# Kernel tuning notes

Measured on AMD Instinct MI355X. Metric: run time of the kernel, lower is better.

Reference implementation:

```python
import jax, jax.numpy as jnp
import numpy as np

NUM_USERS = 100000
NUM_ITEMS = 50000
NUM_NODES = NUM_USERS + NUM_ITEMS
EMBED_DIM = 128
NUM_LAYERS = 3
CONTENT_DIM = 768
NUM_EDGES = 1000000
BATCH = 4096
LAMBDA_CONTENT = 0.1
INIT_STD = 0.1


def setup_inputs() -> dict:
    key = jax.random.key(0)
    ks = jax.random.split(key, 9)
    edge_index = jax.random.randint(ks[0], (2, NUM_EDGES), 0, NUM_NODES, dtype=jnp.int64 if jax.config.jax_enable_x64 else jnp.int32)
    edge_weight = jax.random.uniform(ks[1], (NUM_EDGES,), dtype=jnp.float32)
    batch_users = jax.random.randint(ks[2], (BATCH,), 0, NUM_USERS)
    batch_pos_items = jax.random.randint(ks[3], (BATCH,), 0, NUM_ITEMS)
    batch_neg_items = jax.random.randint(ks[4], (BATCH,), 0, NUM_ITEMS)
    item_content = jax.random.normal(ks[5], (NUM_ITEMS, CONTENT_DIM), dtype=jnp.float32)
    user_emb_w = INIT_STD * jax.random.normal(ks[6], (NUM_USERS, EMBED_DIM), dtype=jnp.float32)
    item_emb_w = INIT_STD * jax.random.normal(ks[7], (NUM_ITEMS, EMBED_DIM), dtype=jnp.float32)
    # nn.Linear(item_content_dim, embed_dim, bias=False): weight [embed_dim, content_dim]
    bound = 1.0 / np.sqrt(CONTENT_DIM)
    content_proj_w = jax.random.uniform(ks[8], (EMBED_DIM, CONTENT_DIM), minval=-bound, maxval=bound, dtype=jnp.float32)
    return {
        'edge_index': edge_index, 'edge_weight': edge_weight,
        'batch_users': batch_users, 'batch_pos_items': batch_pos_items,
        'batch_neg_items': batch_neg_items, 'item_content': item_content,
        'user_emb_w': user_emb_w, 'item_emb_w': item_emb_w,
        'content_proj_w': content_proj_w,
    }


def _lgconv(x, src, dst, ew, num_nodes):
    # PyG LGConv: gcn_norm(add_self_loops=False) then scatter-add at target.
    deg = jax.ops.segment_sum(ew, dst, num_segments=num_nodes)          # [N]
    dinv = jnp.where(deg > 0, jax.lax.rsqrt(deg), 0.0)
    norm = dinv[src] * ew * dinv[dst]                                    # [E]
    return jax.ops.segment_sum(norm[:, None] * x[src], dst, num_segments=num_nodes)


def _propagate(user_emb_w, item_emb_w, src, dst, ew):
    x = jnp.concatenate([user_emb_w, item_emb_w], axis=0)               # [N, D]
    acc = x
    for _ in range(NUM_LAYERS):
        x = _lgconv(x, src, dst, ew, NUM_NODES)
        acc = acc + x
    x_final = acc / (NUM_LAYERS + 1)
    return x_final[:NUM_USERS], x_final[NUM_USERS:]


def reference(edge_index, edge_weight, batch_users, batch_pos_items,
              batch_neg_items, item_content, user_emb_w, item_emb_w,
              content_proj_w):
    src, dst = edge_index[0], edge_index[1]
    u_final, i_final = _propagate(user_emb_w, item_emb_w, src, dst, edge_weight)
    u = u_final[batch_users]
    i_pos = i_final[batch_pos_items]
    i_neg = i_final[batch_neg_items]
    pos_score = jnp.sum(u * i_pos, axis=-1)
    neg_score = jnp.sum(u * i_neg, axis=-1)
    bpr = jnp.mean(jax.nn.softplus(-(pos_score - neg_score)))
    reg = jnp.mean(jnp.sum(u**2, axis=1) + jnp.sum(i_pos**2, axis=1) + jnp.sum(i_neg**2, axis=1)) * 1e-4
    proj = item_content @ content_proj_w.T                              # [I, D]
    align = jnp.mean((i_final - proj) ** 2)
    loss = bpr + reg + LAMBDA_CONTENT * align
    return loss, u_final, i_final
```

## Files before the change

kernel.cpp:

```cpp
#include <hip/hip_runtime.h>
#include <math.h>

#define NU 100000
#define NI 50000
#define NN 150000
#define D 128
#define NE 1000000
#define CD 768
#define BATCH 4096
#define NGEMM 782
#define NGB ((NN + 31) / 32)
#define NK (CD / 64)

typedef short bf16x8 __attribute__((ext_vector_type(8)));
typedef float f32x4 __attribute__((ext_vector_type(4)));

static inline size_t alignup(size_t x, size_t a) { return (x + a - 1) / a * a; }

__device__ inline unsigned short f2bf(float f) {
  unsigned int u = __builtin_bit_cast(unsigned int, f);
  unsigned int r = (u + 0x7fffu + ((u >> 16) & 1u)) >> 16;
  return (unsigned short)r;
}
__device__ inline unsigned int pack2bf(float lo, float hi) {
  return (unsigned int)f2bf(lo) | ((unsigned int)f2bf(hi) << 16);
}
__device__ inline float bflo(unsigned int p) {
  return __builtin_bit_cast(float, p << 16);
}
__device__ inline float bfhi(unsigned int p) {
  return __builtin_bit_cast(float, p & 0xffff0000u);
}

#define ACC8(P, W)                                                        \
  a[0] = fmaf(W, bflo(P.x), a[0]); a[1] = fmaf(W, bfhi(P.x), a[1]);       \
  a[2] = fmaf(W, bflo(P.y), a[2]); a[3] = fmaf(W, bfhi(P.y), a[3]);       \
  a[4] = fmaf(W, bflo(P.z), a[4]); a[5] = fmaf(W, bfhi(P.z), a[5]);       \
  a[6] = fmaf(W, bflo(P.w), a[6]); a[7] = fmaf(W, bfhi(P.w), a[7]);

__device__ __forceinline__ void gather_rows(
    const int* __restrict__ row_ptr, const int* __restrict__ csrc,
    const float* __restrict__ cnorm, const uint4* __restrict__ xin,
    int n, int sub, float* a) {
  int beg = row_ptr[n], end = row_ptr[n + 1];
  int j = beg;
  for (; j + 4 <= end; j += 4) {
    int s0 = csrc[j], s1 = csrc[j + 1], s2 = csrc[j + 2], s3 = csrc[j + 3];
    float w0 = cnorm[j], w1 = cnorm[j + 1], w2 = cnorm[j + 2], w3 = cnorm[j + 3];
    uint4 p0 = xin[(size_t)s0 * 16 + sub];
    uint4 p1 = xin[(size_t)s1 * 16 + sub];
    uint4 p2 = xin[(size_t)s2 * 16 + sub];
    uint4 p3 = xin[(size_t)s3 * 16 + sub];
    ACC8(p0, w0) ACC8(p1, w1) ACC8(p2, w2) ACC8(p3, w3)
  }
  for (; j < end; ++j) {
    int s0 = csrc[j];
    float w0 = cnorm[j];
    uint4 p0 = xin[(size_t)s0 * 16 + sub];
    ACC8(p0, w0)
  }
}

__global__ __launch_bounds__(512) void prep_kernel(
    const int* __restrict__ dst, int* __restrict__ cnt, int* __restrict__ cpos,
    const float* __restrict__ uemb, const float* __restrict__ iemb,
    unsigned int* __restrict__ x0b) {
  int sub = blockIdx.x;
  int half = sub >> 1;
  int tid = threadIdx.x;
  if ((sub & 1) == 0) {
    int i = half * 512 + tid;
    for (; i < NE; i += 1024 * 512)
      cpos[i] = atomicAdd(&cnt[dst[i]], 1);
  } else {
    const size_t XT = (size_t)NN * D / 8;
    size_t t = (size_t)half * 512 + tid;
    for (; t < XT; t += (size_t)1024 * 512) {
      size_t f = t * 8;
      const float* p = (f < (size_t)NU * D) ? (uemb + f) : (iemb + (f - (size_t)NU * D));
      float4 a = *(const float4*)p;
      float4 b = *(const float4*)(p + 4);
      uint4 o;
      o.x = pack2bf(a.x, a.y); o.y = pack2bf(a.z, a.w);
      o.z = pack2bf(b.x, b.y); o.w = pack2bf(b.z, b.w);
      *(uint4*)(x0b + t * 4) = o;
    }
  }
}


__global__ void scan_p1(const int* __restrict__ cnt, int* __restrict__ bsum) {
  __shared__ int s[256];
  int b = blockIdx.x;
  int i = b * 256 + threadIdx.x;
  s[threadIdx.x] = (i < NN) ? cnt[i] : 0;
  __syncthreads();
  for (int off = 128; off; off >>= 1) {
    if (threadIdx.x < off) s[threadIdx.x] += s[threadIdx.x + off];
    __syncthreads();
  }
  if (threadIdx.x == 0) bsum[b] = s[0];
}

__global__ __launch_bounds__(1024) void scan_p2(int* __restrict__ bsum, int nb) {
  __shared__ int s[1024];
  int t = threadIdx.x;
  int v = (t < nb) ? bsum[t] : 0;
  s[t] = v;
  __syncthreads();
  for (int off = 1; off < 1024; off <<= 1) {
    int u = (t >= off) ? s[t - off] : 0;
    __syncthreads();
    s[t] += u;
    __syncthreads();
  }
  if (t < nb) bsum[t] = s[t] - v;
}

__global__ void scan_p3(const int* __restrict__ cnt, const int* __restrict__ bsum,
                        int* __restrict__ row_ptr) {
  __shared__ int s[256];
  int b = blockIdx.x;
  int i = b * 256 + threadIdx.x;
  s[threadIdx.x] = (i < NN) ? cnt[i] : 0;
  __syncthreads();
  for (int off = 1; off < 256; off <<= 1) {
    int t = (threadIdx.x >= off) ? s[threadIdx.x - off] : 0;
    __syncthreads();
    s[threadIdx.x] += t;
    __syncthreads();
  }
  if (i < NN) row_ptr[i + 1] = bsum[b] + s[threadIdx.x];
  if (i == 0) row_ptr[0] = 0;
}

__global__ void fill_kernel(const int* __restrict__ src, const int* __restrict__ dst,
                            const float* __restrict__ ew, const int* __restrict__ row_ptr,
                            const int* __restrict__ cpos, int* __restrict__ csrc,
                            float* __restrict__ cew) {
  int i = blockIdx.x * blockDim.x + threadIdx.x;
  int stride = gridDim.x * blockDim.x;
  for (; i < NE; i += stride) {
    int p = row_ptr[dst[i]] + cpos[i];
    csrc[p] = src[i];
    cew[p] = ew[i];
  }
}

__global__ void degrow_kernel(const int* __restrict__ row_ptr, const float* __restrict__ cew,
                              float* __restrict__ dinv) {
  int n = blockIdx.x * blockDim.x + threadIdx.x;
  if (n >= NN) return;
  int beg = row_ptr[n], end = row_ptr[n + 1];
  float s = 0.f;
  for (int p = beg; p < end; ++p) s += cew[p];
  dinv[n] = (s > 0.f) ? rsqrtf(s) : 0.f;
}

__global__ void norm_kernel(const int* __restrict__ csrc, const float* __restrict__ cew,
                            const float* __restrict__ dinv, float* __restrict__ cnorm) {
  int i = blockIdx.x * blockDim.x + threadIdx.x;
  int stride = gridDim.x * blockDim.x;
  for (; i < NE; i += stride) cnorm[i] = dinv[csrc[i]] * cew[i];
}

__global__ __launch_bounds__(512) void gather1_gemm_kernel(
    const int* __restrict__ row_ptr, const int* __restrict__ csrc,
    const float* __restrict__ cnorm, const float* __restrict__ dinv,
    const uint4* __restrict__ x0b, uint4* __restrict__ y1b,
    const float* __restrict__ W, const float* __restrict__ content,
    uint4* __restrict__ proj) {
  __shared__ unsigned short Asm[64 * 64];
  __shared__ unsigned short Bsm[128 * 64];

  int bid = blockIdx.x;
  int tid = threadIdx.x;

  if (bid >= NGEMM) {
    int wv = tid >> 6, lane = tid & 63;
    int g = lane >> 4, sub = lane & 15;
    int n = (bid - NGEMM) * 32 + wv * 4 + g;
    if (n >= NN) return;
    float a[8] = {0.f, 0.f, 0.f, 0.f, 0.f, 0.f, 0.f, 0.f};
    gather_rows(row_ptr, csrc, cnorm, x0b, n, sub, a);
    float sc = dinv[n];
    uint4 o;
    o.x = pack2bf(a[0] * sc, a[1] * sc);
    o.y = pack2bf(a[2] * sc, a[3] * sc);
    o.z = pack2bf(a[4] * sc, a[5] * sc);
    o.w = pack2bf(a[6] * sc, a[7] * sc);
    y1b[(size_t)n * 16 + sub] = o;
    return;
  }

  int w = tid >> 6, lane = tid & 63;
  int i0 = bid * 64;
  int lrow = lane & 15, kq = lane >> 4;

  f32x4 acc[4];
#pragma unroll
  for (int rt = 0; rt < 4; ++rt) acc[rt] = (f32x4){0.f, 0.f, 0.f, 0.f};

  int sr = tid >> 3, c8 = tid & 7;
  int arow_g = (i0 + sr < NI) ? (i0 + sr) : (NI - 1);
  const float* aG = content + (size_t)arow_g * CD + c8 * 8;
  const float* bG0 = W + (size_t)sr * CD + c8 * 8;
  const float* bG1 = W + (size_t)(sr + 64) * CD + c8 * 8;
  int aoff = (c8 * 16) ^ ((sr & 7) << 4);

  {
    float4 a0 = *(const float4*)(aG);
    float4 a1 = *(const float4*)(aG + 4);
    float4 p0 = *(const float4*)(bG0);
    float4 p1 = *(const float4*)(bG0 + 4);
    float4 q0 = *(const float4*)(bG1);
    float4 q1 = *(const float4*)(bG1 + 4);
    uint4 oa, ob, oc;
    oa.x = pack2bf(a0.x, a0.y); oa.y = pack2bf(a0.z, a0.w);
    oa.z = pack2bf(a1.x, a1.y); oa.w = pack2bf(a1.z, a1.w);
    ob.x = pack2bf(p0.x, p0.y); ob.y = pack2bf(p0.z, p0.w);
    ob.z = pack2bf(p1.x, p1.y); ob.w = pack2bf(p1.z, p1.w);
    oc.x = pack2bf(q0.x, q0.y); oc.y = pack2bf(q0.z, q0.w);
    oc.z = pack2bf(q1.x, q1.y); oc.w = pack2bf(q1.z, q1.w);
    *(uint4*)((char*)Asm + sr * 128 + aoff) = oa;
    *(uint4*)((char*)Bsm + sr * 128 + aoff) = ob;
    *(uint4*)((char*)Bsm + (sr + 64) * 128 + aoff) = oc;
  }
  __syncthreads();

  for (int kk = 0; kk < NK; ++kk) {
    bool more = kk < NK - 1;
    float4 a0, a1, p0, p1, q0, q1;
    if (more) {
      int k0 = (kk + 1) * 64;
      a0 = *(const float4*)(aG + k0);
      a1 = *(const float4*)(aG + k0 + 4);
      p0 = *(const float4*)(bG0 + k0);
      p1 = *(const float4*)(bG0 + k0 + 4);
      q0 = *(const float4*)(bG1 + k0);
      q1 = *(const float4*)(bG1 + k0 + 4);
    }
#pragma unroll
    for (int ks = 0; ks < 2; ++ks) {
      int kbyte = ks * 64 + kq * 16;
      bf16x8 af[4], bfr;
#pragma unroll
      for (int rt = 0; rt < 4; ++rt) {
        int row = rt * 16 + lrow;
        af[rt] = *(const bf16x8*)((char*)Asm + row * 128 + (kbyte ^ ((row & 7) << 4)));
      }
      {
        int row = w * 16 + lrow;
        bfr = *(const bf16x8*)((char*)Bsm + row * 128 + (kbyte ^ ((row & 7) << 4)));
      }
#pragma unroll
      for (int rt = 0; rt < 4; ++rt)
        acc[rt] = __builtin_amdgcn_mfma_f32_16x16x32_bf16(af[rt], bfr, acc[rt], 0, 0, 0);
    }
    __syncthreads();
    if (more) {
      uint4 oa, ob, oc;
      oa.x = pack2bf(a0.x, a0.y); oa.y = pack2bf(a0.z, a0.w);
      oa.z = pack2bf(a1.x, a1.y); oa.w = pack2bf(a1.z, a1.w);
      ob.x = pack2bf(p0.x, p0.y); ob.y = pack2bf(p0.z, p0.w);
      ob.z = pack2bf(p1.x, p1.y); ob.w = pack2bf(p1.z, p1.w);
      oc.x = pack2bf(q0.x, q0.y); oc.y = pack2bf(q0.z, q0.w);
      oc.z = pack2bf(q1.x, q1.y); oc.w = pack2bf(q1.z, q1.w);
      *(uint4*)((char*)Asm + sr * 128 + aoff) = oa;
      *(uint4*)((char*)Bsm + sr * 128 + aoff) = ob;
      *(uint4*)((char*)Bsm + (sr + 64) * 128 + aoff) = oc;
      __syncthreads();
    }
  }

  unsigned short* T = (unsigned short*)Bsm;
  int dcol = w * 16 + lrow;
#pragma unroll
  for (int rt = 0; rt < 4; ++rt)
#pragma unroll
    for (int j = 0; j < 4; ++j)
      T[(rt * 16 + kq * 4 + j) * 128 + dcol] = f2bf(acc[rt][j]);
  __syncthreads();
#pragma unroll
  for (int u0 = 0; u0 < 2; ++u0) {
    int u = u0 * 512 + tid;
    int r = u >> 4, s = u & 15;
    int it = i0 + r;
    if (it < NI) proj[(size_t)it * 16 + s] = ((const uint4*)T)[u];
  }
}

__global__ __launch_bounds__(256) void gather_kernel(
    const int* __restrict__ row_ptr, const int* __restrict__ csrc,
    const float* __restrict__ cnorm, const float* __restrict__ dinv,
    const uint4* __restrict__ xin, uint4* __restrict__ yout) {
  int tid = threadIdx.x;
  int wv = tid >> 6, lane = tid & 63;
  int g = lane >> 4, sub = lane & 15;
  int n = blockIdx.x * 16 + wv * 4 + g;
  if (n >= NN) return;
  float a[8] = {0.f, 0.f, 0.f, 0.f, 0.f, 0.f, 0.f, 0.f};
  gather_rows(row_ptr, csrc, cnorm, xin, n, sub, a);
  float sc = dinv[n];
  uint4 o;
  o.x = pack2bf(a[0] * sc, a[1] * sc);
  o.y = pack2bf(a[2] * sc, a[3] * sc);
  o.z = pack2bf(a[4] * sc, a[5] * sc);
  o.w = pack2bf(a[6] * sc, a[7] * sc);
  yout[(size_t)n * 16 + sub] = o;
}

__global__ __launch_bounds__(256) void final_kernel(
    const int* __restrict__ row_ptr, const int* __restrict__ csrc,
    const float* __restrict__ cnorm, const float* __restrict__ dinv,
    const uint4* __restrict__ x0b, const uint4* __restrict__ y1b,
    const uint4* __restrict__ y2b, const uint4* __restrict__ proj,
    float* __restrict__ OUT, float* __restrict__ partials) {
  __shared__ float wred[4];
  int tid = threadIdx.x;
  int wv = tid >> 6, lane = tid & 63;
  int g = lane >> 4, sub = lane & 15;
  int n = blockIdx.x * 16 + wv * 4 + g;
  if (n >= NN) return;
  float a[8] = {0.f, 0.f, 0.f, 0.f, 0.f, 0.f, 0.f, 0.f};
  gather_rows(row_ptr, csrc, cnorm, y2b, n, sub, a);
  float sc = dinv[n];
  size_t r = (size_t)n * 16 + sub;
  uint4 q0 = x0b[r], q1 = y1b[r], q2 = y2b[r];
  float v[8];
  v[0] = (bflo(q0.x) + bflo(q1.x) + bflo(q2.x) + a[0] * sc) * 0.25f;
  v[1] = (bfhi(q0.x) + bfhi(q1.x) + bfhi(q2.x) + a[1] * sc) * 0.25f;
  v[2] = (bflo(q0.y) + bflo(q1.y) + bflo(q2.y) + a[2] * sc) * 0.25f;
  v[3] = (bfhi(q0.y) + bfhi(q1.y) + bfhi(q2.y) + a[3] * sc) * 0.25f;
  v[4] = (bflo(q0.z) + bflo(q1.z) + bflo(q2.z) + a[4] * sc) * 0.25f;
  v[5] = (bfhi(q0.z) + bfhi(q1.z) + bfhi(q2.z) + a[5] * sc) * 0.25f;
  v[6] = (bflo(q0.w) + bflo(q1.w) + bflo(q2.w) + a[6] * sc) * 0.25f;
  v[7] = (bfhi(q0.w) + bfhi(q1.w) + bfhi(q2.w) + a[7] * sc) * 0.25f;
  float* op = OUT + (size_t)n * D + sub * 8;
#pragma unroll
  for (int k = 0; k < 8; ++k) op[k] = v[k];

  if (blockIdx.x >= (NU / 16)) {
    uint4 pj = proj[(size_t)(n - NU) * 16 + sub];
    float d0 = v[0] - bflo(pj.x), d1 = v[1] - bfhi(pj.x);
    float d2 = v[2] - bflo(pj.y), d3 = v[3] - bfhi(pj.y);
    float d4 = v[4] - bflo(pj.z), d5 = v[5] - bfhi(pj.z);
    float d6 = v[6] - bflo(pj.w), d7 = v[7] - bfhi(pj.w);
    float m = d0 * d0 + d1 * d1 + d2 * d2 + d3 * d3 + d4 * d4 + d5 * d5 + d6 * d6 + d7 * d7;
    for (int off = 32; off; off >>= 1) m += __shfl_down(m, off);
    if (lane == 0) wred[wv] = m;
    __syncthreads();
    if (tid == 0)
      atomicAdd(&partials[blockIdx.x & 255], wred[0] + wred[1] + wred[2] + wred[3]);
  }
}

__global__ __launch_bounds__(256) void loss_batch(
    const int* __restrict__ bu, const int* __restrict__ bp, const int* __restrict__ bn,
    const float* __restrict__ OUT, float* __restrict__ accums) {
  __shared__ float wsp[4], wrg[4];
  int wv = threadIdx.x >> 6, lane = threadIdx.x & 63;
  int gw = blockIdx.x * 4 + wv;
  int nw = gridDim.x * 4;
  float lsp = 0.f, lrg = 0.f;
  for (int b = gw; b < BATCH; b += nw) {
    const float* u = OUT + (size_t)bu[b] * D;
    const float* ip = OUT + ((size_t)NU + bp[b]) * D;
    const float* in_ = OUT + ((size_t)NU + bn[b]) * D;
    float u0 = u[lane], u1 = u[lane + 64];
    float p0 = ip[lane], p1 = ip[lane + 64];
    float n0 = in_[lane], n1 = in_[lane + 64];
    float ps = u0 * p0 + u1 * p1;
    float ns = u0 * n0 + u1 * n1;
    float rg = u0 * u0 + u1 * u1 + p0 * p0 + p1 * p1 + n0 * n0 + n1 * n1;
    for (int off = 32; off; off >>= 1) {
      ps += __shfl_down(ps, off);
      ns += __shfl_down(ns, off);
      rg += __shfl_down(rg, off);
    }
    if (lane == 0) {
      float x = ns - ps;
      lsp += fmaxf(x, 0.f) + log1pf(expf(-fabsf(x)));
      lrg += rg;
    }
  }
  if (lane == 0) { wsp[wv] = lsp; wrg[wv] = lrg; }
  __syncthreads();
  if (threadIdx.x == 0) {
    atomicAdd(&accums[0], wsp[0] + wsp[1] + wsp[2] + wsp[3]);
    atomicAdd(&accums[1], wrg[0] + wrg[1] + wrg[2] + wrg[3]);
  }
}

__global__ void finalize_kernel(const float* __restrict__ accums,
                                const float* __restrict__ partials,
                                float* __restrict__ out0) {
  __shared__ float sm[4];
  int tid = threadIdx.x;
  float v = partials[tid];
  for (int off = 32; off; off >>= 1) v += __shfl_down(v, off);
  if ((tid & 63) == 0) sm[tid >> 6] = v;
  __syncthreads();
  if (tid == 0) {
    float align_sum = sm[0] + sm[1] + sm[2] + sm[3];
    float bpr = accums[0] / (float)BATCH;
    float reg = (accums[1] / (float)BATCH) * 1e-4f;
    float align = align_sum / (float)((size_t)NI * D);
    out0[0] = bpr + reg + 0.1f * align;
  }
}

extern "C" void kernel_launch(void* const* d_in, const int* in_sizes, int n_in,
                              void* d_out, int out_size, void* d_ws, size_t ws_size,
                              hipStream_t stream) {
  const int* edge_index = (const int*)d_in[0];
  const float* ew = (const float*)d_in[1];
  const int* bu = (const int*)d_in[2];
  const int* bp = (const int*)d_in[3];
  const int* bn = (const int*)d_in[4];
  const float* content = (const float*)d_in[5];
  const float* uemb = (const float*)d_in[6];
  const float* iemb = (const float*)d_in[7];
  const float* W = (const float*)d_in[8];
  const int* src = edge_index;
  const int* dst = edge_index + NE;
  float* outf = (float*)d_out;
  float* OUT = outf + 1;

  char* ws = (char*)d_ws;
  size_t off = 0;
  auto alloc = [&](size_t bytes) {
    void* p = ws + off;
    off = alignup(off + bytes, 256);
    return p;
  };
  unsigned int* x0b = (unsigned int*)alloc((size_t)NN * 64 * 4);
  unsigned int* y1b = (unsigned int*)alloc((size_t)NN * 64 * 4);
  unsigned int* y2b = (unsigned int*)alloc((size_t)NN * 64 * 4);
  uint4* proj = (uint4*)alloc((size_t)NI * 16 * 16);
  float* dinv = (float*)alloc((size_t)NN * 4);
  int* cnt = (int*)alloc((size_t)NN * 4);
  int* row_ptr = (int*)alloc((size_t)(NN + 1) * 4);
  int NB = (NN + 255) / 256;
  int* bsum = (int*)alloc((size_t)NB * 4);
  int* cpos = (int*)alloc((size_t)NE * 4);
  int* csrc = (int*)alloc((size_t)NE * 4);
  float* cew = (float*)alloc((size_t)NE * 4);
  float* cnorm = (float*)alloc((size_t)NE * 4);
  float* accums = (float*)alloc(16 + 256 * 4);
  float* partials = accums + 4;

  hipMemsetAsync(cnt, 0, (size_t)NN * 4, stream);
  hipMemsetAsync(accums, 0, 16 + 256 * 4, stream);

  prep_kernel<<<2048, 512, 0, stream>>>(dst, cnt, cpos, uemb, iemb, x0b);
  scan_p1<<<NB, 256, 0, stream>>>(cnt, bsum);
  scan_p2<<<1, 1024, 0, stream>>>(bsum, NB);
  scan_p3<<<NB, 256, 0, stream>>>(cnt, bsum, row_ptr);
  fill_kernel<<<2048, 256, 0, stream>>>(src, dst, ew, row_ptr, cpos, csrc, cew);
  degrow_kernel<<<NB, 256, 0, stream>>>(row_ptr, cew, dinv);
  norm_kernel<<<2048, 256, 0, stream>>>(csrc, cew, dinv, cnorm);

  gather1_gemm_kernel<<<NGEMM + NGB, 512, 0, stream>>>(
      row_ptr, csrc, cnorm, dinv, (const uint4*)x0b, (uint4*)y1b, W, content, proj);
  gather_kernel<<<(NN + 15) / 16, 256, 0, stream>>>(row_ptr, csrc, cnorm, dinv,
                                                    (const uint4*)y1b, (uint4*)y2b);
  final_kernel<<<(NN + 15) / 16, 256, 0, stream>>>(row_ptr, csrc, cnorm, dinv,
                                                   (const uint4*)x0b, (const uint4*)y1b,
                                                   (const uint4*)y2b, proj, OUT, partials);

  loss_batch<<<64, 256, 0, stream>>>(bu, bp, bn, OUT, accums);
  finalize_kernel<<<1, 256, 0, stream>>>(accums, partials, outf);
}
```

Baseline: 347.5 us.

## Interleave edge src/norm into one array, move GEMM into prep kernel, double-buffer LDS

Source indices and normalized weights now live in one interleaved uint2 array, so each gather does one 8-byte load per edge instead of two separate 4-byte loads. The content-projection GEMM blocks move out of the first gather kernel and into the prep kernel, where they run alongside the atomic counting and bf16 conversion. The first propagation layer becomes a plain gather_kernel launch. The GEMM main loop now double-buffers its LDS tiles and needs one barrier per k-step instead of two. The cost is more shared memory per GEMM block, and the prep kernel becomes a larger mixed kernel whose GEMM blocks may delay the scan that follows.

```diff
diff --git a/kernel.cpp b/kernel.cpp
--- a/kernel.cpp
+++ b/kernel.cpp
@@ -9,7 +9,6 @@
 #define CD 768
 #define BATCH 4096
 #define NGEMM 782
-#define NGB ((NN + 31) / 32)
 #define NK (CD / 64)
 
 typedef short bf16x8 __attribute__((ext_vector_type(8)));
@@ -39,24 +38,26 @@
   a[6] = fmaf(W, bflo(P.w), a[6]); a[7] = fmaf(W, bfhi(P.w), a[7]);
 
 __device__ __forceinline__ void gather_rows(
-    const int* __restrict__ row_ptr, const int* __restrict__ csrc,
-    const float* __restrict__ cnorm, const uint4* __restrict__ xin,
-    int n, int sub, float* a) {
+    const int* __restrict__ row_ptr, const uint2* __restrict__ cedge,
+    const uint4* __restrict__ xin, int n, int sub, float* a) {
   int beg = row_ptr[n], end = row_ptr[n + 1];
   int j = beg;
   for (; j + 4 <= end; j += 4) {
-    int s0 = csrc[j], s1 = csrc[j + 1], s2 = csrc[j + 2], s3 = csrc[j + 3];
-    float w0 = cnorm[j], w1 = cnorm[j + 1], w2 = cnorm[j + 2], w3 = cnorm[j + 3];
-    uint4 p0 = xin[(size_t)s0 * 16 + sub];
-    uint4 p1 = xin[(size_t)s1 * 16 + sub];
-    uint4 p2 = xin[(size_t)s2 * 16 + sub];
-    uint4 p3 = xin[(size_t)s3 * 16 + sub];
+    uint2 e0 = cedge[j], e1 = cedge[j + 1], e2 = cedge[j + 2], e3 = cedge[j + 3];
+    uint4 p0 = xin[(size_t)e0.x * 16 + sub];
+    uint4 p1 = xin[(size_t)e1.x * 16 + sub];
+    uint4 p2 = xin[(size_t)e2.x * 16 + sub];
+    uint4 p3 = xin[(size_t)e3.x * 16 + sub];
+    float w0 = __builtin_bit_cast(float, e0.y);
+    float w1 = __builtin_bit_cast(float, e1.y);
+    float w2 = __builtin_bit_cast(float, e2.y);
+    float w3 = __builtin_bit_cast(float, e3.y);
     ACC8(p0, w0) ACC8(p1, w1) ACC8(p2, w2) ACC8(p3, w3)
   }
   for (; j < end; ++j) {
-    int s0 = csrc[j];
-    float w0 = cnorm[j];
-    uint4 p0 = xin[(size_t)s0 * 16 + sub];
+    uint2 e0 = cedge[j];
+    uint4 p0 = xin[(size_t)e0.x * 16 + sub];
+    float w0 = __builtin_bit_cast(float, e0.y);
     ACC8(p0, w0)
   }
 }
@@ -64,132 +65,36 @@
 __global__ __launch_bounds__(512) void prep_kernel(
     const int* __restrict__ dst, int* __restrict__ cnt, int* __restrict__ cpos,
     const float* __restrict__ uemb, const float* __restrict__ iemb,
-    unsigned int* __restrict__ x0b) {
-  int sub = blockIdx.x;
-  int half = sub >> 1;
-  int tid = threadIdx.x;
-  if ((sub & 1) == 0) {
-    int i = half * 512 + tid;
-    for (; i < NE; i += 1024 * 512)
-      cpos[i] = atomicAdd(&cnt[dst[i]], 1);
-  } else {
-    const size_t XT = (size_t)NN * D / 8;
-    size_t t = (size_t)half * 512 + tid;
-    for (; t < XT; t += (size_t)1024 * 512) {
-      size_t f = t * 8;
-      const float* p = (f < (size_t)NU * D) ? (uemb + f) : (iemb + (f - (size_t)NU * D));
-      float4 a = *(const float4*)p;
-      float4 b = *(const float4*)(p + 4);
-      uint4 o;
-      o.x = pack2bf(a.x, a.y); o.y = pack2bf(a.z, a.w);
-      o.z = pack2bf(b.x, b.y); o.w = pack2bf(b.z, b.w);
-      *(uint4*)(x0b + t * 4) = o;
-    }
-  }
-}
-
-
-__global__ void scan_p1(const int* __restrict__ cnt, int* __restrict__ bsum) {
-  __shared__ int s[256];
-  int b = blockIdx.x;
-  int i = b * 256 + threadIdx.x;
-  s[threadIdx.x] = (i < NN) ? cnt[i] : 0;
-  __syncthreads();
-  for (int off = 128; off; off >>= 1) {
-    if (threadIdx.x < off) s[threadIdx.x] += s[threadIdx.x + off];
-    __syncthreads();
-  }
-  if (threadIdx.x == 0) bsum[b] = s[0];
-}
-
-__global__ __launch_bounds__(1024) void scan_p2(int* __restrict__ bsum, int nb) {
-  __shared__ int s[1024];
-  int t = threadIdx.x;
-  int v = (t < nb) ? bsum[t] : 0;
-  s[t] = v;
-  __syncthreads();
-  for (int off = 1; off < 1024; off <<= 1) {
-    int u = (t >= off) ? s[t - off] : 0;
-    __syncthreads();
-    s[t] += u;
-    __syncthreads();
-  }
-  if (t < nb) bsum[t] = s[t] - v;
-}
-
-__global__ void scan_p3(const int* __restrict__ cnt, const int* __restrict__ bsum,
-                        int* __restrict__ row_ptr) {
-  __shared__ int s[256];
-  int b = blockIdx.x;
-  int i = b * 256 + threadIdx.x;
-  s[threadIdx.x] = (i < NN) ? cnt[i] : 0;
-  __syncthreads();
-  for (int off = 1; off < 256; off <<= 1) {
-    int t = (threadIdx.x >= off) ? s[threadIdx.x - off] : 0;
-    __syncthreads();
-    s[threadIdx.x] += t;
-    __syncthreads();
-  }
-  if (i < NN) row_ptr[i + 1] = bsum[b] + s[threadIdx.x];
-  if (i == 0) row_ptr[0] = 0;
-}
-
-__global__ void fill_kernel(const int* __restrict__ src, const int* __restrict__ dst,
-                            const float* __restrict__ ew, const int* __restrict__ row_ptr,
-                            const int* __restrict__ cpos, int* __restrict__ csrc,
-                            float* __restrict__ cew) {
-  int i = blockIdx.x * blockDim.x + threadIdx.x;
-  int stride = gridDim.x * blockDim.x;
-  for (; i < NE; i += stride) {
-    int p = row_ptr[dst[i]] + cpos[i];
-    csrc[p] = src[i];
-    cew[p] = ew[i];
-  }
-}
-
-__global__ void degrow_kernel(const int* __restrict__ row_ptr, const float* __restrict__ cew,
-                              float* __restrict__ dinv) {
-  int n = blockIdx.x * blockDim.x + threadIdx.x;
-  if (n >= NN) return;
-  int beg = row_ptr[n], end = row_ptr[n + 1];
-  float s = 0.f;
-  for (int p = beg; p < end; ++p) s += cew[p];
-  dinv[n] = (s > 0.f) ? rsqrtf(s) : 0.f;
-}
-
-__global__ void norm_kernel(const int* __restrict__ csrc, const float* __restrict__ cew,
-                            const float* __restrict__ dinv, float* __restrict__ cnorm) {
-  int i = blockIdx.x * blockDim.x + threadIdx.x;
-  int stride = gridDim.x * blockDim.x;
-  for (; i < NE; i += stride) cnorm[i] = dinv[csrc[i]] * cew[i];
-}
-
-__global__ __launch_bounds__(512) void gather1_gemm_kernel(
-    const int* __restrict__ row_ptr, const int* __restrict__ csrc,
-    const float* __restrict__ cnorm, const float* __restrict__ dinv,
-    const uint4* __restrict__ x0b, uint4* __restrict__ y1b,
+    unsigned int* __restrict__ x0b,
     const float* __restrict__ W, const float* __restrict__ content,
     uint4* __restrict__ proj) {
-  __shared__ unsigned short Asm[64 * 64];
-  __shared__ unsigned short Bsm[128 * 64];
+  __shared__ unsigned short Asm[2][64 * 64];
+  __shared__ unsigned short Bsm[2][128 * 64];
 
   int bid = blockIdx.x;
   int tid = threadIdx.x;
 
   if (bid >= NGEMM) {
-    int wv = tid >> 6, lane = tid & 63;
-    int g = lane >> 4, sub = lane & 15;
-    int n = (bid - NGEMM) * 32 + wv * 4 + g;
-    if (n >= NN) return;
-    float a[8] = {0.f, 0.f, 0.f, 0.f, 0.f, 0.f, 0.f, 0.f};
-    gather_rows(row_ptr, csrc, cnorm, x0b, n, sub, a);
-    float sc = dinv[n];
-    uint4 o;
-    o.x = pack2bf(a[0] * sc, a[1] * sc);
-    o.y = pack2bf(a[2] * sc, a[3] * sc);
-    o.z = pack2bf(a[4] * sc, a[5] * sc);
-    o.w = pack2bf(a[6] * sc, a[7] * sc);
-    y1b[(size_t)n * 16 + sub] = o;
+    int sub = bid - NGEMM;
+    int half = sub >> 1;
+    if ((sub & 1) == 0) {
+      int i = half * 512 + tid;
+      for (; i < NE; i += 1024 * 512)
+        cpos[i] = atomicAdd(&cnt[dst[i]], 1);
+    } else {
+      const size_t XT = (size_t)NN * D / 8;
+      size_t t = (size_t)half * 512 + tid;
+      for (; t < XT; t += (size_t)1024 * 512) {
+        size_t f = t * 8;
+        const float* p = (f < (size_t)NU * D) ? (uemb + f) : (iemb + (f - (size_t)NU * D));
+        float4 a = *(const float4*)p;
+        float4 b = *(const float4*)(p + 4);
+        uint4 o;
+        o.x = pack2bf(a.x, a.y); o.y = pack2bf(a.z, a.w);
+        o.z = pack2bf(b.x, b.y); o.w = pack2bf(b.z, b.w);
+        *(uint4*)(x0b + t * 4) = o;
+      }
+    }
     return;
   }
 
@@ -222,13 +127,14 @@
     ob.z = pack2bf(p1.x, p1.y); ob.w = pack2bf(p1.z, p1.w);
     oc.x = pack2bf(q0.x, q0.y); oc.y = pack2bf(q0.z, q0.w);
     oc.z = pack2bf(q1.x, q1.y); oc.w = pack2bf(q1.z, q1.w);
-    *(uint4*)((char*)Asm + sr * 128 + aoff) = oa;
-    *(uint4*)((char*)Bsm + sr * 128 + aoff) = ob;
-    *(uint4*)((char*)Bsm + (sr + 64) * 128 + aoff) = oc;
-  }
-  __syncthreads();
+    *(uint4*)((char*)Asm[0] + sr * 128 + aoff) = oa;
+    *(uint4*)((char*)Bsm[0] + sr * 128 + aoff) = ob;
+    *(uint4*)((char*)Bsm[0] + (sr + 64) * 128 + aoff) = oc;
+  }
 
   for (int kk = 0; kk < NK; ++kk) {
+    __syncthreads();
+    int cur = kk & 1, nxt = cur ^ 1;
     bool more = kk < NK - 1;
     float4 a0, a1, p0, p1, q0, q1;
     if (more) {
@@ -247,17 +153,16 @@
 #pragma unroll
       for (int rt = 0; rt < 4; ++rt) {
         int row = rt * 16 + lrow;
-        af[rt] = *(const bf16x8*)((char*)Asm + row * 128 + (kbyte ^ ((row & 7) << 4)));
+        af[rt] = *(const bf16x8*)((char*)Asm[cur] + row * 128 + (kbyte ^ ((row & 7) << 4)));
       }
       {
         int row = w * 16 + lrow;
-        bfr = *(const bf16x8*)((char*)Bsm + row * 128 + (kbyte ^ ((row & 7) << 4)));
+        bfr = *(const bf16x8*)((char*)Bsm[cur] + row * 128 + (kbyte ^ ((row & 7) << 4)));
       }
 #pragma unroll
       for (int rt = 0; rt < 4; ++rt)
         acc[rt] = __builtin_amdgcn_mfma_f32_16x16x32_bf16(af[rt], bfr, acc[rt], 0, 0, 0);
     }
-    __syncthreads();
     if (more) {
       uint4 oa, ob, oc;
       oa.x = pack2bf(a0.x, a0.y); oa.y = pack2bf(a0.z, a0.w);
@@ -266,14 +171,14 @@
       ob.z = pack2bf(p1.x, p1.y); ob.w = pack2bf(p1.z, p1.w);
       oc.x = pack2bf(q0.x, q0.y); oc.y = pack2bf(q0.z, q0.w);
       oc.z = pack2bf(q1.x, q1.y); oc.w = pack2bf(q1.z, q1.w);
-      *(uint4*)((char*)Asm + sr * 128 + aoff) = oa;
-      *(uint4*)((char*)Bsm + sr * 128 + aoff) = ob;
-      *(uint4*)((char*)Bsm + (sr + 64) * 128 + aoff) = oc;
-      __syncthreads();
-    }
-  }
-
-  unsigned short* T = (unsigned short*)Bsm;
+      *(uint4*)((char*)Asm[nxt] + sr * 128 + aoff) = oa;
+      *(uint4*)((char*)Bsm[nxt] + sr * 128 + aoff) = ob;
+      *(uint4*)((char*)Bsm[nxt] + (sr + 64) * 128 + aoff) = oc;
+    }
+  }
+
+  __syncthreads();
+  unsigned short* T = (unsigned short*)Asm;
   int dcol = w * 16 + lrow;
 #pragma unroll
   for (int rt = 0; rt < 4; ++rt)
@@ -290,17 +195,97 @@
   }
 }
 
+
+__global__ void scan_p1(const int* __restrict__ cnt, int* __restrict__ bsum) {
+  __shared__ int s[256];
+  int b = blockIdx.x;
+  int i = b * 256 + threadIdx.x;
+  s[threadIdx.x] = (i < NN) ? cnt[i] : 0;
+  __syncthreads();
+  for (int off = 128; off; off >>= 1) {
+    if (threadIdx.x < off) s[threadIdx.x] += s[threadIdx.x + off];
+    __syncthreads();
+  }
+  if (threadIdx.x == 0) bsum[b] = s[0];
+}
+
+__global__ __launch_bounds__(1024) void scan_p2(int* __restrict__ bsum, int nb) {
+  __shared__ int s[1024];
+  int t = threadIdx.x;
+  int v = (t < nb) ? bsum[t] : 0;
+  s[t] = v;
+  __syncthreads();
+  for (int off = 1; off < 1024; off <<= 1) {
+    int u = (t >= off) ? s[t - off] : 0;
+    __syncthreads();
+    s[t] += u;
+    __syncthreads();
+  }
+  if (t < nb) bsum[t] = s[t] - v;
+}
+
+__global__ void scan_p3(const int* __restrict__ cnt, const int* __restrict__ bsum,
+                        int* __restrict__ row_ptr) {
+  __shared__ int s[256];
+  int b = blockIdx.x;
+  int i = b * 256 + threadIdx.x;
+  s[threadIdx.x] = (i < NN) ? cnt[i] : 0;
+  __syncthreads();
+  for (int off = 1; off < 256; off <<= 1) {
+    int t = (threadIdx.x >= off) ? s[threadIdx.x - off] : 0;
+    __syncthreads();
+    s[threadIdx.x] += t;
+    __syncthreads();
+  }
+  if (i < NN) row_ptr[i + 1] = bsum[b] + s[threadIdx.x];
+  if (i == 0) row_ptr[0] = 0;
+}
+
+__global__ void fill_kernel(const int* __restrict__ src, const int* __restrict__ dst,
+                            const float* __restrict__ ew, const int* __restrict__ row_ptr,
+                            const int* __restrict__ cpos, uint2* __restrict__ cedge) {
+  int i = blockIdx.x * blockDim.x + threadIdx.x;
+  int stride = gridDim.x * blockDim.x;
+  for (; i < NE; i += stride) {
+    int p = row_ptr[dst[i]] + cpos[i];
+    uint2 e;
+    e.x = (unsigned int)src[i];
+    e.y = __builtin_bit_cast(unsigned int, ew[i]);
+    cedge[p] = e;
+  }
+}
+
+__global__ void degrow_kernel(const int* __restrict__ row_ptr, const uint2* __restrict__ cedge,
+                              float* __restrict__ dinv) {
+  int n = blockIdx.x * blockDim.x + threadIdx.x;
+  if (n >= NN) return;
+  int beg = row_ptr[n], end = row_ptr[n + 1];
+  float s = 0.f;
+  for (int p = beg; p < end; ++p) s += __builtin_bit_cast(float, cedge[p].y);
+  dinv[n] = (s > 0.f) ? rsqrtf(s) : 0.f;
+}
+
+__global__ void norm_kernel(uint2* __restrict__ cedge, const float* __restrict__ dinv) {
+  int i = blockIdx.x * blockDim.x + threadIdx.x;
+  int stride = gridDim.x * blockDim.x;
+  for (; i < NE; i += stride) {
+    uint2 e = cedge[i];
+    float nm = dinv[e.x] * __builtin_bit_cast(float, e.y);
+    cedge[i].y = __builtin_bit_cast(unsigned int, nm);
+  }
+}
+
 __global__ __launch_bounds__(256) void gather_kernel(
-    const int* __restrict__ row_ptr, const int* __restrict__ csrc,
-    const float* __restrict__ cnorm, const float* __restrict__ dinv,
-    const uint4* __restrict__ xin, uint4* __restrict__ yout) {
+    const int* __restrict__ row_ptr, const uint2* __restrict__ cedge,
+    const float* __restrict__ dinv, const uint4* __restrict__ xin,
+    uint4* __restrict__ yout) {
   int tid = threadIdx.x;
   int wv = tid >> 6, lane = tid & 63;
   int g = lane >> 4, sub = lane & 15;
   int n = blockIdx.x * 16 + wv * 4 + g;
   if (n >= NN) return;
   float a[8] = {0.f, 0.f, 0.f, 0.f, 0.f, 0.f, 0.f, 0.f};
-  gather_rows(row_ptr, csrc, cnorm, xin, n, sub, a);
+  gather_rows(row_ptr, cedge, xin, n, sub, a);
   float sc = dinv[n];
   uint4 o;
   o.x = pack2bf(a[0] * sc, a[1] * sc);
@@ -311,11 +296,11 @@
 }
 
 __global__ __launch_bounds__(256) void final_kernel(
-    const int* __restrict__ row_ptr, const int* __restrict__ csrc,
-    const float* __restrict__ cnorm, const float* __restrict__ dinv,
-    const uint4* __restrict__ x0b, const uint4* __restrict__ y1b,
-    const uint4* __restrict__ y2b, const uint4* __restrict__ proj,
-    float* __restrict__ OUT, float* __restrict__ partials) {
+    const int* __restrict__ row_ptr, const uint2* __restrict__ cedge,
+    const float* __restrict__ dinv, const uint4* __restrict__ x0b,
+    const uint4* __restrict__ y1b, const uint4* __restrict__ y2b,
+    const uint4* __restrict__ proj, float* __restrict__ OUT,
+    float* __restrict__ partials) {
   __shared__ float wred[4];
   int tid = threadIdx.x;
   int wv = tid >> 6, lane = tid & 63;
@@ -323,7 +308,7 @@
   int n = blockIdx.x * 16 + wv * 4 + g;
   if (n >= NN) return;
   float a[8] = {0.f, 0.f, 0.f, 0.f, 0.f, 0.f, 0.f, 0.f};
-  gather_rows(row_ptr, csrc, cnorm, y2b, n, sub, a);
+  gather_rows(row_ptr, cedge, y2b, n, sub, a);
   float sc = dinv[n];
   size_t r = (size_t)n * 16 + sub;
   uint4 q0 = x0b[r], q1 = y1b[r], q2 = y2b[r];
@@ -444,30 +429,27 @@
   int NB = (NN + 255) / 256;
   int* bsum = (int*)alloc((size_t)NB * 4);
   int* cpos = (int*)alloc((size_t)NE * 4);
-  int* csrc = (int*)alloc((size_t)NE * 4);
-  float* cew = (float*)alloc((size_t)NE * 4);
-  float* cnorm = (float*)alloc((size_t)NE * 4);
+  uint2* cedge = (uint2*)alloc((size_t)NE * 8);
   float* accums = (float*)alloc(16 + 256 * 4);
   float* partials = accums + 4;
 
   hipMemsetAsync(cnt, 0, (size_t)NN * 4, stream);
   hipMemsetAsync(accums, 0, 16 + 256 * 4, stream);
 
-  prep_kernel<<<2048, 512, 0, stream>>>(dst, cnt, cpos, uemb, iemb, x0b);
+  prep_kernel<<<NGEMM + 2048, 512, 0, stream>>>(dst, cnt, cpos, uemb, iemb, x0b, W, content, proj);
   scan_p1<<<NB, 256, 0, stream>>>(cnt, bsum);
   scan_p2<<<1, 1024, 0, stream>>>(bsum, NB);
   scan_p3<<<NB, 256, 0, stream>>>(cnt, bsum, row_ptr);
-  fill_kernel<<<2048, 256, 0, stream>>>(src, dst, ew, row_ptr, cpos, csrc, cew);
-  degrow_kernel<<<NB, 256, 0, stream>>>(row_ptr, cew, dinv);
-  norm_kernel<<<2048, 256, 0, stream>>>(csrc, cew, dinv, cnorm);
-
-  gather1_gemm_kernel<<<NGEMM + NGB, 512, 0, stream>>>(
-      row_ptr, csrc, cnorm, dinv, (const uint4*)x0b, (uint4*)y1b, W, content, proj);
-  gather_kernel<<<(NN + 15) / 16, 256, 0, stream>>>(row_ptr, csrc, cnorm, dinv,
-                                                    (const uint4*)y1b, (uint4*)y2b);
-  final_kernel<<<(NN + 15) / 16, 256, 0, stream>>>(row_ptr, csrc, cnorm, dinv,
-                                                   (const uint4*)x0b, (const uint4*)y1b,
-                                                   (const uint4*)y2b, proj, OUT, partials);
+  fill_kernel<<<2048, 256, 0, stream>>>(src, dst, ew, row_ptr, cpos, cedge);
+  degrow_kernel<<<NB, 256, 0, stream>>>(row_ptr, cedge, dinv);
+  norm_kernel<<<2048, 256, 0, stream>>>(cedge, dinv);
+
+  int LB = (NN + 15) / 16;
+  gather_kernel<<<LB, 256, 0, stream>>>(row_ptr, cedge, dinv, (const uint4*)x0b, (uint4*)y1b);
+  gather_kernel<<<LB, 256, 0, stream>>>(row_ptr, cedge, dinv, (const uint4*)y1b, (uint4*)y2b);
+  final_kernel<<<LB, 256, 0, stream>>>(row_ptr, cedge, dinv,
+                                       (const uint4*)x0b, (const uint4*)y1b, (const uint4*)y2b,
+                                       proj, OUT, partials);
 
   loss_batch<<<64, 256, 0, stream>>>(bu, bp, bn, OUT, accums);
   finalize_kernel<<<1, 256, 0, stream>>>(accums, partials, outf);
```

Measured after the change: 322.2 us. -7.3%, faster.
